# Performance work log

Hardware: AMD Instinct MI355X
Metric: run time of the kernel (lower is better)

## Reference

```python
import jax, jax.numpy as jnp
import numpy as np

D_MODEL = 768
D_HID = 3072
D_OUT = 768
N_EXP = 8
TOP_K = 2
B, S = 2, 2048
LN_EPS = 1e-5


def setup_inputs() -> dict:
    key = jax.random.key(0)
    ks = jax.random.split(key, 10)
    sc_in = 1.0 / np.sqrt(D_MODEL)
    sc_hid = 1.0 / np.sqrt(D_HID)
    return {
        "x": jax.random.normal(ks[0], (B, S, D_MODEL), dtype=jnp.float32),
        "Wr": jax.random.normal(ks[1], (D_MODEL, N_EXP), dtype=jnp.float32) * sc_in,
        "br": jnp.zeros((N_EXP,), dtype=jnp.float32),
        "W1": jax.random.normal(ks[2], (N_EXP, D_MODEL, D_HID), dtype=jnp.float32) * sc_in,
        "b1": jnp.zeros((N_EXP, D_HID), dtype=jnp.float32),
        "W2": jax.random.normal(ks[3], (N_EXP, D_HID, D_OUT), dtype=jnp.float32) * sc_hid,
        "b2": jnp.zeros((N_EXP, D_OUT), dtype=jnp.float32),
        "ln_g": jnp.ones((D_OUT,), dtype=jnp.float32),
        "ln_b": jnp.zeros((D_OUT,), dtype=jnp.float32),
    }


def reference(x, Wr, br, W1, b1, W2, b2, ln_g, ln_b):
    # --- top-k router ---
    logits = jnp.einsum("bsd,de->bse", x, Wr) + br          # [B,S,E]
    probs = jax.nn.softmax(logits, axis=-1)
    top_vals, top_idx = jax.lax.top_k(probs, TOP_K)          # [B,S,K]
    routing_weights = top_vals / jnp.sum(top_vals, axis=-1, keepdims=True)

    # per-token weight given to each expert (0 if not selected)
    onehot = jax.nn.one_hot(top_idx, N_EXP, dtype=x.dtype)   # [B,S,K,E]
    expert_weights = jnp.einsum("bsk,bske->bse", routing_weights, onehot)

    # --- dense per-expert FFN over ALL tokens (faithful to source loop) ---
    h = jax.nn.gelu(jnp.einsum("bsd,edh->besh", x, W1) + b1[None, :, None, :])
    y = jnp.einsum("besh,eho->beso", h, W2) + b2[None, :, None, :]  # [B,E,S,O]

    # weighted combine
    out = jnp.einsum("beso,bse->bso", y, expert_weights)     # [B,S,O]

    # --- output LayerNorm ---
    mu = jnp.mean(out, axis=-1, keepdims=True)
    var = jnp.mean(jnp.square(out - mu), axis=-1, keepdims=True)
    out = (out - mu) * jax.lax.rsqrt(var + LN_EPS) * ln_g + ln_b
    return out
```

## Files before the change

### kernel.cpp

```cpp
#include <hip/hip_runtime.h>
#include <hip/hip_bf16.h>

#define TOKENS 4096
#define DMODEL 768
#define DHID   3072
#define NEXP   8
#define MAXT   72

typedef __bf16 bf16x8 __attribute__((ext_vector_type(8)));
typedef float  f32x4  __attribute__((ext_vector_type(4)));
typedef unsigned short ushort_t;

#define VMCNT(n) asm volatile("s_waitcnt vmcnt(" #n ")" ::: "memory")

__device__ __forceinline__ void wg_barrier() {
    asm volatile("" ::: "memory");
    __builtin_amdgcn_s_barrier();
    asm volatile("" ::: "memory");
}

__device__ __forceinline__ float gelu_tanh(float x) {
    float z = 0.7978845608028654f * (x + 0.044715f * x * x * x);
    float t = 1.0f - 2.0f / (__expf(2.0f * z) + 1.0f);
    return 0.5f * x * (1.0f + t);
}

__device__ __forceinline__ float bf2f(ushort_t u) {
    unsigned v = ((unsigned)u) << 16;
    return __builtin_bit_cast(float, v);
}

__device__ __forceinline__ void gload16(const void* g, void* l) {
    __builtin_amdgcn_global_load_lds((const __attribute__((address_space(1))) void*)g,
                                     (__attribute__((address_space(3))) void*)l, 16, 0, 0);
}

__global__ void k_transpose_cvt(const float* __restrict__ in, ushort_t* __restrict__ out,
                                int R, int C) {
    __shared__ float tile[64 * 68];
    const int bx = blockIdx.x, by = blockIdx.y, bz = blockIdx.z;
    const float* ip = in + (size_t)bz * R * C;
    ushort_t* op = out + (size_t)bz * R * C;
    const int tid = threadIdx.x;
    {
        const int cq = tid & 15, rg = tid >> 4;
#pragma unroll
        for (int i = 0; i < 4; ++i) {
            int rl = rg + i * 16;
            float4 v = *(const float4*)(ip + (size_t)(by * 64 + rl) * C + bx * 64 + cq * 4);
            *(float4*)(&tile[rl * 68 + cq * 4]) = v;
        }
    }
    __syncthreads();
    {
        const int rq = tid & 15, cg = tid >> 4;
#pragma unroll
        for (int i = 0; i < 4; ++i) {
            int cl = cg + i * 16;
            ushort4 o;
            o.x = __builtin_bit_cast(ushort_t, (__bf16)tile[(rq * 4 + 0) * 68 + cl]);
            o.y = __builtin_bit_cast(ushort_t, (__bf16)tile[(rq * 4 + 1) * 68 + cl]);
            o.z = __builtin_bit_cast(ushort_t, (__bf16)tile[(rq * 4 + 2) * 68 + cl]);
            o.w = __builtin_bit_cast(ushort_t, (__bf16)tile[(rq * 4 + 3) * 68 + cl]);
            *(ushort4*)(op + (size_t)(bx * 64 + cl) * R + by * 64 + rq * 4) = o;
        }
    }
}

__launch_bounds__(256)
__global__ void k_router(const float* __restrict__ x, const float* __restrict__ Wr,
                         const float* __restrict__ br, int* __restrict__ cnt,
                         int* __restrict__ tok, int* __restrict__ slot,
                         float* __restrict__ wslot, ushort_t* __restrict__ xb) {
    __shared__ float WrT[NEXP * DMODEL];
    __shared__ int   te0[32], te1[32];
    __shared__ int   lcnt[NEXP], gbase[NEXP];

    const int tid = threadIdx.x;
    const int wv = tid >> 6, lane = tid & 63;

#pragma unroll
    for (int i = 0; i < 6; ++i) {
        int idx4 = i * 256 + tid;
        float4 v = ((const float4*)Wr)[idx4];
        int flat = idx4 * 4;
        int d = flat >> 3, e0 = flat & 7;
        WrT[(e0 + 0) * DMODEL + d] = v.x;
        WrT[(e0 + 1) * DMODEL + d] = v.y;
        WrT[(e0 + 2) * DMODEL + d] = v.z;
        WrT[(e0 + 3) * DMODEL + d] = v.w;
    }
    if (tid < NEXP) lcnt[tid] = 0;
    float brv[8];
#pragma unroll
    for (int e = 0; e < 8; ++e) brv[e] = br[e];
    __syncthreads();

#pragma unroll 1
    for (int it = 0; it < 8; ++it) {
        int t = blockIdx.x * 32 + wv * 8 + it;
        const float* xr = x + (size_t)t * DMODEL;
        float4 xv[3];
#pragma unroll
        for (int j = 0; j < 3; ++j) xv[j] = *(const float4*)(xr + (j * 64 + lane) * 4);
#pragma unroll
        for (int j = 0; j < 3; ++j) {
            int base = (j * 64 + lane) * 4;
            ushort4 o;
            o.x = __builtin_bit_cast(ushort_t, (__bf16)xv[j].x);
            o.y = __builtin_bit_cast(ushort_t, (__bf16)xv[j].y);
            o.z = __builtin_bit_cast(ushort_t, (__bf16)xv[j].z);
            o.w = __builtin_bit_cast(ushort_t, (__bf16)xv[j].w);
            *(ushort4*)(xb + (size_t)t * DMODEL + base) = o;
        }
        float lg[8];
#pragma unroll
        for (int e = 0; e < 8; ++e) {
            float s = 0.f;
#pragma unroll
            for (int j = 0; j < 3; ++j) {
                const float4 wv4 = *(const float4*)(&WrT[e * DMODEL + (j * 64 + lane) * 4]);
                s += xv[j].x * wv4.x;
                s += xv[j].y * wv4.y;
                s += xv[j].z * wv4.z;
                s += xv[j].w * wv4.w;
            }
#pragma unroll
            for (int o = 32; o > 0; o >>= 1) s += __shfl_xor(s, o);
            lg[e] = s + brv[e];
        }
        if (lane == 0) {
            int e0 = 0; float b0 = lg[0];
#pragma unroll
            for (int e = 1; e < 8; ++e) if (lg[e] > b0) { b0 = lg[e]; e0 = e; }
            int e1 = -1; float b1v = -1e30f;
#pragma unroll
            for (int e = 0; e < 8; ++e) if (e != e0 && lg[e] > b1v) { b1v = lg[e]; e1 = e; }
            float w0 = 1.f / (1.f + __expf(b1v - b0));
            float w1 = 1.f - w0;
            int lt = wv * 8 + it;
            te0[lt] = e0; te1[lt] = e1;
            wslot[2 * t] = w0; wslot[2 * t + 1] = w1;
        }
    }
    __syncthreads();

    int myE = 0, myPos = 0, myTok = 0, myK = 0;
    if (tid < 64) {
        int lt = tid >> 1; myK = tid & 1;
        myE = myK ? te1[lt] : te0[lt];
        myTok = blockIdx.x * 32 + lt;
        myPos = atomicAdd(&lcnt[myE], 1);
    }
    __syncthreads();
    if (tid < NEXP) gbase[tid] = atomicAdd(&cnt[tid], lcnt[tid]);
    __syncthreads();
    if (tid < 64) {
        int g = gbase[myE] + myPos;
        tok[myE * TOKENS + g] = myTok;
        slot[myE * TOKENS + g] = 2 * myTok + myK;
    }
}

__global__ void k_sched(const int* __restrict__ cnt, int* __restrict__ sch) {
    if (threadIdx.x == 0) {
        int base = 0, n = 0;
        for (int e = 0; e < NEXP; ++e) {
            sch[2 + e] = base;
            int ce = cnt[e];
            for (int m = 0; m < ce; m += 128) sch[16 + n++] = (e << 20) | m;
            base += ce;
        }
        sch[0] = n;
    }
}

template<bool STAGE1>
__launch_bounds__(256, 2)
__global__ void k_gemm8(const ushort_t* __restrict__ Abase, const int* __restrict__ tok,
                        const int* __restrict__ slot, const ushort_t* __restrict__ Wb,
                        const float* __restrict__ bias, void* __restrict__ outp,
                        const int* __restrict__ cnt, const int* __restrict__ sch) {
    constexpr int KR  = STAGE1 ? DMODEL : DHID;
    constexpr int NCn = STAGE1 ? DHID : DMODEL;
    constexpr int NT  = STAGE1 ? (DMODEL / 64) : (DHID / 2 / 64);

    const int bx = blockIdx.x;
    const int tile = (bx & 7) * 9 + (bx >> 3);
    const int nT = sch[0];
    if (tile >= nT) return;
    const int ent = sch[16 + tile];
    const int e = ent >> 20, m0 = ent & 0xFFFFF;
    const int ce = cnt[e];
    const int bH = sch[2 + e];
    const int n0 = blockIdx.y * 128;
    const int kbase = STAGE1 ? 0 : (int)blockIdx.z * (DHID / 2);

    __shared__ ushort_t lds[32768];
    char* ldsB = (char*)lds;

    const int tid = threadIdx.x, lane = tid & 63, w = tid >> 6;
    const int wm = w >> 1, wn = w & 1;
    const int wmBase = wm * 64, wnBase = wn * 64;
    const int fr = lane & 15, fg = lane >> 4;

    const ushort_t* aPtr[2];
    const ushort_t* bPtr[2];
#pragma unroll
    for (int i = 0; i < 2; ++i) {
        int row = (w * 2 + i) * 16 + (lane >> 2);
        int gblk = (lane & 3) ^ ((row >> 1) & 3);
        int gi = min(m0 + row, ce - 1);
        size_t ar = STAGE1 ? (size_t)tok[e * TOKENS + gi] : (size_t)(bH + gi);
        aPtr[i] = Abase + ar * KR + kbase + gblk * 8;
        bPtr[i] = Wb + ((size_t)e * NCn + n0 + row) * KR + kbase + gblk * 8;
    }

    auto stage4 = [&](int kt1, int boff) {
#pragma unroll
        for (int i = 0; i < 2; ++i) {
            const ushort_t* a = aPtr[i] + kt1 * 64;
            const ushort_t* b = bPtr[i] + kt1 * 64;
            gload16(a,      ldsB + boff +         w * 2048 + i * 1024);
            gload16(a + 32, ldsB + boff +  8192 + w * 2048 + i * 1024);
            gload16(b,      ldsB + boff + 16384 + w * 2048 + i * 1024);
            gload16(b + 32, ldsB + boff + 24576 + w * 2048 + i * 1024);
        }
    };

    const int arow0 = wmBase + fr;
    const int abase = arow0 * 64 + ((fg ^ ((arow0 >> 1) & 3)) << 4);
    const int brow0 = wnBase + fr;
    const int bbase = 16384 + brow0 * 64 + ((fg ^ ((brow0 >> 1) & 3)) << 4);

    f32x4 acc[4][4] = {};

    stage4(0, 0);
    VMCNT(0);
    wg_barrier();

#pragma unroll 1
    for (int kt = 0; kt < NT; ++kt) {
        const int boff = (kt & 1) * 32768;
        const char* bufL = ldsB + boff;
        if (kt + 1 < NT) stage4(kt + 1, boff ^ 32768);

        bf16x8 a0[4], b0[4], a1[4], b1f[4];
#pragma unroll
        for (int i = 0; i < 4; ++i) {
            a0[i]  = *(const bf16x8*)(bufL + abase + i * 1024);
            b0[i]  = *(const bf16x8*)(bufL + bbase + i * 1024);
            a1[i]  = *(const bf16x8*)(bufL + abase + 8192 + i * 1024);
            b1f[i] = *(const bf16x8*)(bufL + bbase + 8192 + i * 1024);
        }
        __builtin_amdgcn_s_setprio(1);
#pragma unroll
        for (int mi = 0; mi < 4; ++mi)
#pragma unroll
            for (int ni = 0; ni < 4; ++ni)
                acc[mi][ni] = __builtin_amdgcn_mfma_f32_16x16x32_bf16(a0[mi], b0[ni], acc[mi][ni], 0, 0, 0);
#pragma unroll
        for (int mi = 0; mi < 4; ++mi)
#pragma unroll
            for (int ni = 0; ni < 4; ++ni)
                acc[mi][ni] = __builtin_amdgcn_mfma_f32_16x16x32_bf16(a1[mi], b1f[ni], acc[mi][ni], 0, 0, 0);
        __builtin_amdgcn_s_setprio(0);

        VMCNT(0);
        wg_barrier();
    }

    float bv[4];
#pragma unroll
    for (int ni = 0; ni < 4; ++ni)
        bv[ni] = bias[e * NCn + n0 + wnBase + ni * 16 + fr];
#pragma unroll
    for (int mi = 0; mi < 4; ++mi) {
#pragma unroll
        for (int r4 = 0; r4 < 4; ++r4) {
            int gi = m0 + wmBase + mi * 16 + fg * 4 + r4;
            if (gi < ce) {
                if constexpr (STAGE1) {
                    size_t orow = (size_t)(bH + gi);
#pragma unroll
                    for (int ni = 0; ni < 4; ++ni) {
                        int col = n0 + wnBase + ni * 16 + fr;
                        float v = gelu_tanh(acc[mi][ni][r4] + bv[ni]);
                        ((ushort_t*)outp)[orow * DHID + col] =
                            __builtin_bit_cast(ushort_t, (__bf16)v);
                    }
                } else {
                    size_t orow = (size_t)blockIdx.z * 8192 + (size_t)slot[e * TOKENS + gi];
                    float badd = (blockIdx.z == 0) ? 1.f : 0.f;
#pragma unroll
                    for (int ni = 0; ni < 4; ++ni) {
                        int col = n0 + wnBase + ni * 16 + fr;
                        float v = acc[mi][ni][r4] + badd * bv[ni];
                        ((ushort_t*)outp)[orow * DMODEL + col] =
                            __builtin_bit_cast(ushort_t, (__bf16)v);
                    }
                }
            }
        }
    }
}

__global__ void k_ln(const ushort_t* __restrict__ Y2, const float* __restrict__ wslot,
                     const float* __restrict__ g, const float* __restrict__ b,
                     float* __restrict__ out) {
    int wv = threadIdx.x >> 6, lane = threadIdx.x & 63;
    int t = blockIdx.x * 4 + wv;
    const ushort_t* r00 = Y2 + (size_t)(2 * t) * DMODEL;
    const ushort_t* r01 = Y2 + (size_t)(8192 + 2 * t) * DMODEL;
    const ushort_t* r10 = r00 + DMODEL;
    const ushort_t* r11 = r01 + DMODEL;
    float w0 = wslot[2 * t], w1 = wslot[2 * t + 1];
    float4 v[3];
    float s = 0.f, ss = 0.f;
#pragma unroll
    for (int j = 0; j < 3; ++j) {
        int base = (j * 64 + lane) * 4;
        ushort4 a0 = *(const ushort4*)(r00 + base);
        ushort4 a1 = *(const ushort4*)(r01 + base);
        ushort4 c0 = *(const ushort4*)(r10 + base);
        ushort4 c1 = *(const ushort4*)(r11 + base);
        float4 c;
        c.x = w0 * (bf2f(a0.x) + bf2f(a1.x)) + w1 * (bf2f(c0.x) + bf2f(c1.x));
        c.y = w0 * (bf2f(a0.y) + bf2f(a1.y)) + w1 * (bf2f(c0.y) + bf2f(c1.y));
        c.z = w0 * (bf2f(a0.z) + bf2f(a1.z)) + w1 * (bf2f(c0.z) + bf2f(c1.z));
        c.w = w0 * (bf2f(a0.w) + bf2f(a1.w)) + w1 * (bf2f(c0.w) + bf2f(c1.w));
        v[j] = c;
        s  += c.x + c.y + c.z + c.w;
        ss += c.x * c.x + c.y * c.y + c.z * c.z + c.w * c.w;
    }
#pragma unroll
    for (int o = 32; o > 0; o >>= 1) { s += __shfl_xor(s, o); ss += __shfl_xor(ss, o); }
    float mu = s * (1.f / 768.f);
    float var = ss * (1.f / 768.f) - mu * mu;
    float inv = rsqrtf(var + 1e-5f);
    float* row = out + (size_t)t * DMODEL;
#pragma unroll
    for (int j = 0; j < 3; ++j) {
        int base = (j * 64 + lane) * 4;
        float4 gv = *(const float4*)(g + base);
        float4 bv = *(const float4*)(b + base);
        float4 o4;
        o4.x = (v[j].x - mu) * inv * gv.x + bv.x;
        o4.y = (v[j].y - mu) * inv * gv.y + bv.y;
        o4.z = (v[j].z - mu) * inv * gv.z + bv.z;
        o4.w = (v[j].w - mu) * inv * gv.w + bv.w;
        *(float4*)(row + base) = o4;
    }
}

extern "C" void kernel_launch(void* const* d_in, const int* in_sizes, int n_in,
                              void* d_out, int out_size, void* d_ws, size_t ws_size,
                              hipStream_t stream) {
    const float* x    = (const float*)d_in[0];
    const float* Wr   = (const float*)d_in[1];
    const float* br   = (const float*)d_in[2];
    const float* W1   = (const float*)d_in[3];
    const float* b1   = (const float*)d_in[4];
    const float* W2   = (const float*)d_in[5];
    const float* b2   = (const float*)d_in[6];
    const float* ln_g = (const float*)d_in[7];
    const float* ln_b = (const float*)d_in[8];
    float* out = (float*)d_out;

    char* ws = (char*)d_ws;
    int*      cnt   = (int*)(ws + 0);
    int*      sch   = (int*)(ws + 64);
    int*      tok   = (int*)(ws + 4096);
    int*      slot  = (int*)(ws + 135168);
    float*    wslot = (float*)(ws + 266240);
    ushort_t* xb    = (ushort_t*)(ws + 327680);
    ushort_t* W1t   = (ushort_t*)(ws + 6619136);
    ushort_t* W2t   = (ushort_t*)(ws + 44367872);
    ushort_t* H     = (ushort_t*)(ws + 82116608);
    ushort_t* Y2    = (ushort_t*)(ws + 132448256);

    hipMemsetAsync(cnt, 0, 32, stream);

    k_transpose_cvt<<<dim3(DHID / 64, DMODEL / 64, NEXP), dim3(256), 0, stream>>>(W1, W1t, DMODEL, DHID);
    k_transpose_cvt<<<dim3(DMODEL / 64, DHID / 64, NEXP), dim3(256), 0, stream>>>(W2, W2t, DHID, DMODEL);
    k_router<<<dim3(TOKENS / 32), dim3(256), 0, stream>>>(x, Wr, br, cnt, tok, slot, wslot, xb);
    k_sched<<<dim3(1), dim3(64), 0, stream>>>(cnt, sch);

    k_gemm8<true><<<dim3(MAXT, DHID / 128, 1), dim3(256), 0, stream>>>(
        xb, tok, slot, W1t, b1, H, cnt, sch);
    k_gemm8<false><<<dim3(MAXT, DMODEL / 128, 2), dim3(256), 0, stream>>>(
        H, tok, slot, W2t, b2, Y2, cnt, sch);

    k_ln<<<dim3(TOKENS / 4), dim3(256), 0, stream>>>(Y2, wslot, ln_g, ln_b, out);
}
```

Baseline: 208.0 us.

## Widen grouped GEMM tile to 128x256 with triple-buffered BK=32 LDS pipeline

Both expert GEMM stages move from 128x128 tiles with a double-buffered BK=64 loop to 128x256 tiles with a three-buffer BK=32 pipeline that prefetches two K-steps ahead and waits with a partial vmcnt. Each wave now holds a 4x8 accumulator block, which raises MFMA work per LDS fragment load and halves the number of column blocks. The aim is to reuse A-tile loads more and to hide global-load latency better. The cost is higher register pressure, which may lower occupancy under launch_bounds(256,2), and fewer workgroups, especially in stage 2 where DMODEL/256 gives only 3 column blocks.

```diff
diff --git a/kernel.cpp b/kernel.cpp
--- a/kernel.cpp
+++ b/kernel.cpp
@@ -183,7 +183,8 @@
                         const int* __restrict__ cnt, const int* __restrict__ sch) {
     constexpr int KR  = STAGE1 ? DMODEL : DHID;
     constexpr int NCn = STAGE1 ? DHID : DMODEL;
-    constexpr int NT  = STAGE1 ? (DMODEL / 64) : (DHID / 2 / 64);
+    constexpr int NT  = STAGE1 ? (DMODEL / 32) : (DHID / 2 / 32);
+    constexpr int BUFB = 24576;
 
     const int bx = blockIdx.x;
     const int tile = (bx & 7) * 9 + (bx >> 3);
@@ -193,98 +194,95 @@
     const int e = ent >> 20, m0 = ent & 0xFFFFF;
     const int ce = cnt[e];
     const int bH = sch[2 + e];
-    const int n0 = blockIdx.y * 128;
+    const int n0 = blockIdx.y * 256;
     const int kbase = STAGE1 ? 0 : (int)blockIdx.z * (DHID / 2);
 
-    __shared__ ushort_t lds[32768];
+    __shared__ ushort_t lds[3 * BUFB / 2];
     char* ldsB = (char*)lds;
 
     const int tid = threadIdx.x, lane = tid & 63, w = tid >> 6;
     const int wm = w >> 1, wn = w & 1;
-    const int wmBase = wm * 64, wnBase = wn * 64;
     const int fr = lane & 15, fg = lane >> 4;
 
-    const ushort_t* aPtr[2];
-    const ushort_t* bPtr[2];
+    const ushort_t* aSrc[2]; int aDst[2];
 #pragma unroll
     for (int i = 0; i < 2; ++i) {
-        int row = (w * 2 + i) * 16 + (lane >> 2);
-        int gblk = (lane & 3) ^ ((row >> 1) & 3);
+        int s = i * 256 + tid;
+        int row = s >> 2;
+        int blk = (s & 3) ^ ((row >> 1) & 3);
         int gi = min(m0 + row, ce - 1);
         size_t ar = STAGE1 ? (size_t)tok[e * TOKENS + gi] : (size_t)(bH + gi);
-        aPtr[i] = Abase + ar * KR + kbase + gblk * 8;
-        bPtr[i] = Wb + ((size_t)e * NCn + n0 + row) * KR + kbase + gblk * 8;
-    }
-
-    auto stage4 = [&](int kt1, int boff) {
-#pragma unroll
-        for (int i = 0; i < 2; ++i) {
-            const ushort_t* a = aPtr[i] + kt1 * 64;
-            const ushort_t* b = bPtr[i] + kt1 * 64;
-            gload16(a,      ldsB + boff +         w * 2048 + i * 1024);
-            gload16(a + 32, ldsB + boff +  8192 + w * 2048 + i * 1024);
-            gload16(b,      ldsB + boff + 16384 + w * 2048 + i * 1024);
-            gload16(b + 32, ldsB + boff + 24576 + w * 2048 + i * 1024);
-        }
+        aSrc[i] = Abase + ar * KR + kbase + blk * 8;
+        aDst[i] = s * 16;
+    }
+    const ushort_t* bSrc[4]; int bDst[4];
+#pragma unroll
+    for (int i = 0; i < 4; ++i) {
+        int s = i * 256 + tid;
+        int row = s >> 2;
+        int blk = (s & 3) ^ ((row >> 1) & 3);
+        bSrc[i] = Wb + ((size_t)e * NCn + n0 + row) * KR + kbase + blk * 8;
+        bDst[i] = 8192 + s * 16;
+    }
+
+    auto stage = [&](int kt1, char* db) {
+#pragma unroll
+        for (int i = 0; i < 2; ++i) gload16(aSrc[i] + kt1 * 32, db + aDst[i]);
+#pragma unroll
+        for (int i = 0; i < 4; ++i) gload16(bSrc[i] + kt1 * 32, db + bDst[i]);
     };
 
-    const int arow0 = wmBase + fr;
+    const int arow0 = wm * 64 + fr;
     const int abase = arow0 * 64 + ((fg ^ ((arow0 >> 1) & 3)) << 4);
-    const int brow0 = wnBase + fr;
-    const int bbase = 16384 + brow0 * 64 + ((fg ^ ((brow0 >> 1) & 3)) << 4);
-
-    f32x4 acc[4][4] = {};
-
-    stage4(0, 0);
-    VMCNT(0);
+    const int brow0 = wn * 128 + fr;
+    const int bbase = 8192 + brow0 * 64 + ((fg ^ ((brow0 >> 1) & 3)) << 4);
+
+    f32x4 acc[4][8] = {};
+
+    stage(0, ldsB);
+    stage(1, ldsB + BUFB);
+    VMCNT(6);
     wg_barrier();
 
 #pragma unroll 1
     for (int kt = 0; kt < NT; ++kt) {
-        const int boff = (kt & 1) * 32768;
-        const char* bufL = ldsB + boff;
-        if (kt + 1 < NT) stage4(kt + 1, boff ^ 32768);
-
-        bf16x8 a0[4], b0[4], a1[4], b1f[4];
-#pragma unroll
-        for (int i = 0; i < 4; ++i) {
-            a0[i]  = *(const bf16x8*)(bufL + abase + i * 1024);
-            b0[i]  = *(const bf16x8*)(bufL + bbase + i * 1024);
-            a1[i]  = *(const bf16x8*)(bufL + abase + 8192 + i * 1024);
-            b1f[i] = *(const bf16x8*)(bufL + bbase + 8192 + i * 1024);
-        }
+        const char* bufL = ldsB + (kt % 3) * BUFB;
+        bf16x8 a[4], b[8];
+#pragma unroll
+        for (int mi = 0; mi < 4; ++mi) a[mi] = *(const bf16x8*)(bufL + abase + mi * 1024);
+#pragma unroll
+        for (int ni = 0; ni < 8; ++ni) b[ni] = *(const bf16x8*)(bufL + bbase + ni * 1024);
+
+        if (kt + 2 < NT) stage(kt + 2, ldsB + ((kt + 2) % 3) * BUFB);
+
         __builtin_amdgcn_s_setprio(1);
 #pragma unroll
         for (int mi = 0; mi < 4; ++mi)
 #pragma unroll
-            for (int ni = 0; ni < 4; ++ni)
-                acc[mi][ni] = __builtin_amdgcn_mfma_f32_16x16x32_bf16(a0[mi], b0[ni], acc[mi][ni], 0, 0, 0);
-#pragma unroll
-        for (int mi = 0; mi < 4; ++mi)
-#pragma unroll
-            for (int ni = 0; ni < 4; ++ni)
-                acc[mi][ni] = __builtin_amdgcn_mfma_f32_16x16x32_bf16(a1[mi], b1f[ni], acc[mi][ni], 0, 0, 0);
+            for (int ni = 0; ni < 8; ++ni)
+                acc[mi][ni] = __builtin_amdgcn_mfma_f32_16x16x32_bf16(a[mi], b[ni], acc[mi][ni], 0, 0, 0);
         __builtin_amdgcn_s_setprio(0);
 
-        VMCNT(0);
+        if (kt + 2 < NT) { VMCNT(6); }
+        else            { VMCNT(0); }
         wg_barrier();
     }
 
-    float bv[4];
-#pragma unroll
-    for (int ni = 0; ni < 4; ++ni)
-        bv[ni] = bias[e * NCn + n0 + wnBase + ni * 16 + fr];
+    float bv[8];
+#pragma unroll
+    for (int ni = 0; ni < 8; ++ni)
+        bv[ni] = bias[e * NCn + n0 + wn * 128 + ni * 16 + fr];
 #pragma unroll
     for (int mi = 0; mi < 4; ++mi) {
 #pragma unroll
         for (int r4 = 0; r4 < 4; ++r4) {
-            int gi = m0 + wmBase + mi * 16 + fg * 4 + r4;
+            int gi = m0 + wm * 64 + mi * 16 + fg * 4 + r4;
             if (gi < ce) {
                 if constexpr (STAGE1) {
                     size_t orow = (size_t)(bH + gi);
 #pragma unroll
-                    for (int ni = 0; ni < 4; ++ni) {
-                        int col = n0 + wnBase + ni * 16 + fr;
+                    for (int ni = 0; ni < 8; ++ni) {
+                        int col = n0 + wn * 128 + ni * 16 + fr;
                         float v = gelu_tanh(acc[mi][ni][r4] + bv[ni]);
                         ((ushort_t*)outp)[orow * DHID + col] =
                             __builtin_bit_cast(ushort_t, (__bf16)v);
@@ -293,8 +291,8 @@
                     size_t orow = (size_t)blockIdx.z * 8192 + (size_t)slot[e * TOKENS + gi];
                     float badd = (blockIdx.z == 0) ? 1.f : 0.f;
 #pragma unroll
-                    for (int ni = 0; ni < 4; ++ni) {
-                        int col = n0 + wnBase + ni * 16 + fr;
+                    for (int ni = 0; ni < 8; ++ni) {
+                        int col = n0 + wn * 128 + ni * 16 + fr;
                         float v = acc[mi][ni][r4] + badd * bv[ni];
                         ((ushort_t*)outp)[orow * DMODEL + col] =
                             __builtin_bit_cast(ushort_t, (__bf16)v);
@@ -386,9 +384,9 @@
     k_router<<<dim3(TOKENS / 32), dim3(256), 0, stream>>>(x, Wr, br, cnt, tok, slot, wslot, xb);
     k_sched<<<dim3(1), dim3(64), 0, stream>>>(cnt, sch);
 
-    k_gemm8<true><<<dim3(MAXT, DHID / 128, 1), dim3(256), 0, stream>>>(
+    k_gemm8<true><<<dim3(MAXT, DHID / 256, 1), dim3(256), 0, stream>>>(
         xb, tok, slot, W1t, b1, H, cnt, sch);
-    k_gemm8<false><<<dim3(MAXT, DMODEL / 128, 2), dim3(256), 0, stream>>>(
+    k_gemm8<false><<<dim3(MAXT, DMODEL / 256, 2), dim3(256), 0, stream>>>(
         H, tok, slot, W2t, b2, Y2, cnt, sch);
 
     k_ln<<<dim3(TOKENS / 4), dim3(256), 0, stream>>>(Y2, wslot, ln_g, ln_b, out);
```

After: 207.1 us. About the same (-0.5%).

## Load A fragments directly to registers, stage only B in LDS

Applied to the files above, without the earlier changes.

The grouped expert GEMM no longer stages the A (token activation) tile through LDS. Each wave loads its own A fragments straight from global memory into registers, double-buffered through two register sets in a manually unrolled two-step loop. Only the weight tile B still goes through LDS, which halves shared memory to 32 KB and removes the LDS write and read traffic for A. In exchange, A fragments are duplicated across the two N-waves, global loads become gathered per-row reads, and register pressure rises under the 2-blocks-per-SM launch bound.

```diff
diff --git a/kernel.cpp b/kernel.cpp
--- a/kernel.cpp
+++ b/kernel.cpp
@@ -174,6 +174,41 @@
         sch[0] = n;
     }
 }
+
+
+#define BODY(kt_, AC, AN)                                                              \
+    {                                                                                  \
+        char* bufc = ldsB + ((kt_) & 1) * 16384;                                       \
+        if ((kt_) + 1 < NT) {                                                          \
+            char* bufn = ldsB + (((kt_) + 1) & 1) * 16384;                             \
+            _Pragma("unroll")                                                          \
+            for (int i_ = 0; i_ < 4; ++i_)                                             \
+                gload16(bSrc[i_] + ((kt_) + 1) * 64, bufn + bDst[i_]);                 \
+            _Pragma("unroll")                                                          \
+            for (int mi_ = 0; mi_ < 4; ++mi_) {                                        \
+                AN[mi_]     = *(const bf16x8*)(aRowP[mi_] + ((kt_) + 1) * 64);         \
+                AN[4 + mi_] = *(const bf16x8*)(aRowP[mi_] + ((kt_) + 1) * 64 + 32);    \
+            }                                                                          \
+        }                                                                              \
+        bf16x8 bf0[4], bf1[4];                                                         \
+        _Pragma("unroll")                                                              \
+        for (int ni_ = 0; ni_ < 4; ++ni_) {                                            \
+            bf0[ni_] = *(const bf16x8*)(bufc + bOff[ni_]);                             \
+            bf1[ni_] = *(const bf16x8*)(bufc + 8192 + bOff[ni_]);                      \
+        }                                                                              \
+        __builtin_amdgcn_s_setprio(1);                                                 \
+        _Pragma("unroll")                                                              \
+        for (int mi_ = 0; mi_ < 4; ++mi_) {                                            \
+            _Pragma("unroll")                                                          \
+            for (int ni_ = 0; ni_ < 4; ++ni_) {                                        \
+                acc[mi_][ni_] = __builtin_amdgcn_mfma_f32_16x16x32_bf16(AC[mi_], bf0[ni_], acc[mi_][ni_], 0, 0, 0); \
+                acc[mi_][ni_] = __builtin_amdgcn_mfma_f32_16x16x32_bf16(AC[4 + mi_], bf1[ni_], acc[mi_][ni_], 0, 0, 0); \
+            }                                                                          \
+        }                                                                              \
+        __builtin_amdgcn_s_setprio(0);                                                 \
+        VMCNT(0);                                                                      \
+        wg_barrier();                                                                  \
+    }
 
 template<bool STAGE1>
 __launch_bounds__(256, 2)
@@ -196,95 +231,73 @@
     const int n0 = blockIdx.y * 128;
     const int kbase = STAGE1 ? 0 : (int)blockIdx.z * (DHID / 2);
 
-    __shared__ ushort_t lds[32768];
+    __shared__ ushort_t lds[16384];
     char* ldsB = (char*)lds;
 
     const int tid = threadIdx.x, lane = tid & 63, w = tid >> 6;
     const int wm = w >> 1, wn = w & 1;
-    const int wmBase = wm * 64, wnBase = wn * 64;
     const int fr = lane & 15, fg = lane >> 4;
 
-    const ushort_t* aPtr[2];
-    const ushort_t* bPtr[2];
-#pragma unroll
-    for (int i = 0; i < 2; ++i) {
-        int row = (w * 2 + i) * 16 + (lane >> 2);
-        int gblk = (lane & 3) ^ ((row >> 1) & 3);
-        int gi = min(m0 + row, ce - 1);
+    const ushort_t* aRowP[4];
+#pragma unroll
+    for (int mi = 0; mi < 4; ++mi) {
+        int gi = min(m0 + wm * 64 + mi * 16 + fr, ce - 1);
         size_t ar = STAGE1 ? (size_t)tok[e * TOKENS + gi] : (size_t)(bH + gi);
-        aPtr[i] = Abase + ar * KR + kbase + gblk * 8;
-        bPtr[i] = Wb + ((size_t)e * NCn + n0 + row) * KR + kbase + gblk * 8;
-    }
-
-    auto stage4 = [&](int kt1, int boff) {
-#pragma unroll
-        for (int i = 0; i < 2; ++i) {
-            const ushort_t* a = aPtr[i] + kt1 * 64;
-            const ushort_t* b = bPtr[i] + kt1 * 64;
-            gload16(a,      ldsB + boff +         w * 2048 + i * 1024);
-            gload16(a + 32, ldsB + boff +  8192 + w * 2048 + i * 1024);
-            gload16(b,      ldsB + boff + 16384 + w * 2048 + i * 1024);
-            gload16(b + 32, ldsB + boff + 24576 + w * 2048 + i * 1024);
-        }
-    };
-
-    const int arow0 = wmBase + fr;
-    const int abase = arow0 * 64 + ((fg ^ ((arow0 >> 1) & 3)) << 4);
-    const int brow0 = wnBase + fr;
-    const int bbase = 16384 + brow0 * 64 + ((fg ^ ((brow0 >> 1) & 3)) << 4);
+        aRowP[mi] = Abase + ar * KR + kbase + fg * 8;
+    }
+
+    const ushort_t* bSrc[4]; int bDst[4];
+#pragma unroll
+    for (int i = 0; i < 4; ++i) {
+        int s = i * 256 + tid;
+        int ks = s >> 9;
+        int row = (s & 511) >> 2;
+        int blk = (s & 3) ^ ((row >> 1) & 3);
+        bSrc[i] = Wb + ((size_t)e * NCn + n0 + row) * KR + kbase + ks * 32 + blk * 8;
+        bDst[i] = s * 16;
+    }
+
+    int bOff[4];
+#pragma unroll
+    for (int ni = 0; ni < 4; ++ni) {
+        int row = wn * 64 + ni * 16 + fr;
+        bOff[ni] = row * 64 + ((fg ^ ((row >> 1) & 3)) << 4);
+    }
 
     f32x4 acc[4][4] = {};
-
-    stage4(0, 0);
+    bf16x8 aC[8], aN[8];
+
+#pragma unroll
+    for (int i = 0; i < 4; ++i) gload16(bSrc[i], ldsB + bDst[i]);
+#pragma unroll
+    for (int mi = 0; mi < 4; ++mi) {
+        aC[mi]     = *(const bf16x8*)(aRowP[mi]);
+        aC[4 + mi] = *(const bf16x8*)(aRowP[mi] + 32);
+    }
     VMCNT(0);
     wg_barrier();
 
 #pragma unroll 1
-    for (int kt = 0; kt < NT; ++kt) {
-        const int boff = (kt & 1) * 32768;
-        const char* bufL = ldsB + boff;
-        if (kt + 1 < NT) stage4(kt + 1, boff ^ 32768);
-
-        bf16x8 a0[4], b0[4], a1[4], b1f[4];
-#pragma unroll
-        for (int i = 0; i < 4; ++i) {
-            a0[i]  = *(const bf16x8*)(bufL + abase + i * 1024);
-            b0[i]  = *(const bf16x8*)(bufL + bbase + i * 1024);
-            a1[i]  = *(const bf16x8*)(bufL + abase + 8192 + i * 1024);
-            b1f[i] = *(const bf16x8*)(bufL + bbase + 8192 + i * 1024);
-        }
-        __builtin_amdgcn_s_setprio(1);
-#pragma unroll
-        for (int mi = 0; mi < 4; ++mi)
-#pragma unroll
-            for (int ni = 0; ni < 4; ++ni)
-                acc[mi][ni] = __builtin_amdgcn_mfma_f32_16x16x32_bf16(a0[mi], b0[ni], acc[mi][ni], 0, 0, 0);
-#pragma unroll
-        for (int mi = 0; mi < 4; ++mi)
-#pragma unroll
-            for (int ni = 0; ni < 4; ++ni)
-                acc[mi][ni] = __builtin_amdgcn_mfma_f32_16x16x32_bf16(a1[mi], b1f[ni], acc[mi][ni], 0, 0, 0);
-        __builtin_amdgcn_s_setprio(0);
-
-        VMCNT(0);
-        wg_barrier();
+    for (int kt = 0; kt < NT; kt += 2) {
+        BODY(kt, aC, aN)
+        BODY(kt + 1, aN, aC)
     }
 
     float bv[4];
 #pragma unroll
     for (int ni = 0; ni < 4; ++ni)
-        bv[ni] = bias[e * NCn + n0 + wnBase + ni * 16 + fr];
+        bv[ni] = bias[e * NCn + n0 + wn * 64 + ni * 16 + fr];
 #pragma unroll
     for (int mi = 0; mi < 4; ++mi) {
 #pragma unroll
         for (int r4 = 0; r4 < 4; ++r4) {
-            int gi = m0 + wmBase + mi * 16 + fg * 4 + r4;
+            int gi = m0 + wm * 64 + mi * 16 + fg * 4 + r4;
             if (gi < ce) {
                 if constexpr (STAGE1) {
                     size_t orow = (size_t)(bH + gi);
 #pragma unroll
                     for (int ni = 0; ni < 4; ++ni) {
-                        int col = n0 + wnBase + ni * 16 + fr;
+                        int col = n0 + wn * 64 + ni * 16 + fr;
                         float v = gelu_tanh(acc[mi][ni][r4] + bv[ni]);
                         ((ushort_t*)outp)[orow * DHID + col] =
                             __builtin_bit_cast(ushort_t, (__bf16)v);
@@ -294,7 +307,7 @@
                     float badd = (blockIdx.z == 0) ? 1.f : 0.f;
 #pragma unroll
                     for (int ni = 0; ni < 4; ++ni) {
-                        int col = n0 + wnBase + ni * 16 + fr;
+                        int col = n0 + wn * 64 + ni * 16 + fr;
                         float v = acc[mi][ni][r4] + badd * bv[ni];
                         ((ushort_t*)outp)[orow * DMODEL + col] =
                             __builtin_bit_cast(ushort_t, (__bf16)v);
```

Result: slower. 314.6 us (+51.3%).
